# Optimization experiments

Hardware: AMD Instinct MI355X
Metric: run time of the kernel (lower is better)

Reference implementation:

```python
import jax, jax.numpy as jnp
import numpy as np

HIDDEN = 1024
B, S = 4, 2048


def setup_inputs() -> dict:
    key = jax.random.key(0)
    ks = jax.random.split(key, 8)
    scale = 1.0 / np.sqrt(HIDDEN)
    return {
        "hidden_states": jax.random.normal(ks[0], (B, S, HIDDEN), dtype=jnp.float32),
        "attention_mask": jnp.zeros((B, S, S), dtype=jnp.float32),
        "Wq": jax.random.normal(ks[1], (HIDDEN, HIDDEN), dtype=jnp.float32) * scale,
        "bq": jnp.zeros((HIDDEN,), dtype=jnp.float32),
        "Wk": jax.random.normal(ks[2], (HIDDEN, HIDDEN), dtype=jnp.float32) * scale,
        "bk": jnp.zeros((HIDDEN,), dtype=jnp.float32),
        "Wv": jax.random.normal(ks[3], (HIDDEN, HIDDEN), dtype=jnp.float32) * scale,
        "bv": jnp.zeros((HIDDEN,), dtype=jnp.float32),
    }


def reference(hidden_states, attention_mask, Wq, bq, Wk, bk, Wv, bv):
    # Dense projections (note: no head split in the original module)
    q = jnp.einsum('bsd,de->bse', hidden_states, Wq) + bq  # [B,S,H]
    k = jnp.einsum('bsd,de->bse', hidden_states, Wk) + bk
    v = jnp.einsum('bsd,de->bse', hidden_states, Wv) + bv
    # scores scaled by sqrt(hidden_size) (not per-head dim), per the source
    inv_scale = 1.0 / jnp.sqrt(jnp.asarray(q.shape[-1], dtype=q.dtype))
    scores = jnp.einsum('bqd,bkd->bqk', q, k) * inv_scale  # [B,S,S]
    scores = scores + attention_mask
    weights = jax.nn.softmax(scores, axis=-1)
    # dropout is identity (training=False)
    out = jnp.einsum('bqk,bkd->bqd', weights, v)  # [B,S,H]
    return out
```

## Files before the change

kernel.cpp:

```cpp
#include <hip/hip_runtime.h>
#include <stdint.h>

typedef __attribute__((ext_vector_type(8))) short short8;
typedef __attribute__((ext_vector_type(8))) unsigned short u16x8;
typedef __attribute__((ext_vector_type(4))) float f32x4;

__device__ __forceinline__ uint16_t f2bf(float x) {
  uint32_t u = __float_as_uint(x);
  uint32_t r = (u + 0x7FFFu + ((u >> 16) & 1u)) >> 16;
  return (uint16_t)r;
}
__device__ __forceinline__ float bf2f(uint16_t x) {
  return __uint_as_float(((uint32_t)x) << 16);
}

__device__ __forceinline__ void gl_lds16(const uint16_t* g, void* l) {
  __builtin_amdgcn_global_load_lds(
      (const __attribute__((address_space(1))) void*)g,
      (__attribute__((address_space(3))) void*)l, 16, 0, 0);
}


__global__ __launch_bounds__(256) void cvt_f32_to_bf16(const float* __restrict__ in,
                                                       uint16_t* __restrict__ out) {
  long i = ((long)blockIdx.x * 256 + threadIdx.x) * 8;
  f32x4 v0 = *(const f32x4*)(in + i);
  f32x4 v1 = *(const f32x4*)(in + i + 4);
  u16x8 o;
  o[0] = f2bf(v0[0]); o[1] = f2bf(v0[1]); o[2] = f2bf(v0[2]); o[3] = f2bf(v0[3]);
  o[4] = f2bf(v1[0]); o[5] = f2bf(v1[1]); o[6] = f2bf(v1[2]); o[7] = f2bf(v1[3]);
  *(u16x8*)(out + i) = o;
}

__global__ __launch_bounds__(64) void cvt_w_transpose(const float* __restrict__ W0,
                                                      const float* __restrict__ W1,
                                                      const float* __restrict__ W2,
                                                      uint16_t* __restrict__ WT) {
  const int z = blockIdx.z;
  const float* W = (z == 0) ? W0 : ((z == 1) ? W1 : W2);
  uint16_t* out = WT + (long)z * 1024 * 1024;
  const int n = blockIdx.x * 64 + threadIdx.x;
  const int k0 = blockIdx.y * 128;
  for (int kk = 0; kk < 128; kk += 8) {
    u16x8 o;
#pragma unroll
    for (int j = 0; j < 8; j++) o[j] = f2bf(W[(long)(k0 + kk + j) * 1024 + n]);
    *(u16x8*)(out + (long)n * 1024 + k0 + kk) = o;
  }
}

__global__ __launch_bounds__(256) void transpose_v(const uint16_t* __restrict__ V,
                                                   uint16_t* __restrict__ Vt) {
  __shared__ uint16_t tile[64][66];
  const int b = blockIdx.z;
  const int s0 = blockIdx.x * 64, d0 = blockIdx.y * 64;
  const int t = threadIdx.x;
  const int r = t >> 3, c = (t & 7) * 8;
  const uint16_t* Vb = V + (long)b * 2048 * 1024;
#pragma unroll
  for (int j = 0; j < 2; j++) {
    u16x8 v = *(const u16x8*)(Vb + (long)(s0 + r + 32 * j) * 1024 + d0 + c);
#pragma unroll
    for (int i = 0; i < 8; i++) tile[r + 32 * j][c + i] = v[i];
  }
  __syncthreads();
  uint16_t* Vtb = Vt + (long)b * 1024 * 2048;
#pragma unroll
  for (int j = 0; j < 2; j++) {
    const int d = r + 32 * j;
    u16x8 o;
#pragma unroll
    for (int i = 0; i < 8; i++) o[i] = tile[c + i][d];
    *(u16x8*)(Vtb + (long)(d0 + d) * 2048 + s0 + c) = o;
  }
}

template <int MODE, int AI>
__global__ __launch_bounds__(512, 2) void gemmX(
    const uint16_t* __restrict__ Abase, long sAz,
    const uint16_t* __restrict__ Bbase, long sBz,
    int K, int N,
    char* __restrict__ Cbase, long sCz,
    const float* __restrict__ e0, const float* __restrict__ e1,
    const float* __restrict__ e2,
    const float* __restrict__ maskb, long sMz, float scale,
    float* __restrict__ lsum) {
  constexpr int BM = AI * 32;
  constexpr int ABYTES = BM * 128;
  constexpr int BUFB = ABYTES + 32768;
  __shared__ __align__(16) char lds[2 * BUFB];
  const int t = threadIdx.x;
  const int lane = t & 63;
  const int w = t >> 6;
  const int bm = blockIdx.x, bn = blockIdx.y, bz = blockIdx.z;
  const uint16_t* A = (const uint16_t*)((const char*)Abase + (long)bz * sAz);
  const uint16_t* B = (const uint16_t*)((const char*)Bbase + (long)bz * sBz);

  const int srow = t >> 3;
  const int scol = ((((t & 7) * 16) ^ ((srow & 7) << 4)) >> 1);
  const uint16_t* gA[4];
  const uint16_t* gB[4];
#pragma unroll
  for (int s = 0; s < 4; s++) {
    gA[s] = A + (long)(bm * BM + (s % (AI / 2)) * 64 + srow) * K + scol;
    gB[s] = B + (long)(bn * 256 + s * 64 + srow) * K + scol;
  }

  const int wm = w >> 2, wn = w & 3;
  const int fr = lane & 15, kg = lane >> 4;
  const int X = (fr & 7) << 4;
  const int aRow = (wm * (AI * 16) + fr) * 128 + kg * 16;
  const int bRow = (wn * 64 + fr) * 128 + kg * 16;

  f32x4 acc[AI][4];
#pragma unroll
  for (int i = 0; i < AI; i++)
#pragma unroll
    for (int j = 0; j < 4; j++) acc[i][j] = (f32x4){0.f, 0.f, 0.f, 0.f};

  short8 aR[4][2], bR[4][2];
  const int NT = K >> 6;

#define ARD(off, i, ks) (*(const short8*)(lds + (off) + ((aRow + (i) * 2048 + (ks) * 64) ^ X)))
#define BRD(off, j, ks) (*(const short8*)(lds + ABYTES + (off) + ((bRow + (j) * 2048 + (ks) * 64) ^ X)))
#define STG_A01(off, ko) { gl_lds16(gA[0] + (ko), lds + (off) + w * 1024); \
                           gl_lds16(gA[1] + (ko), lds + (off) + 8192 + w * 1024); }
#define STG_A23(off, ko) { gl_lds16(gA[2] + (ko), lds + (off) + 16384 + w * 1024); \
                           gl_lds16(gA[3] + (ko), lds + (off) + 24576 + w * 1024); }
#define STG_B01(off, ko) { gl_lds16(gB[0] + (ko), lds + ABYTES + (off) + w * 1024); \
                           gl_lds16(gB[1] + (ko), lds + ABYTES + (off) + 8192 + w * 1024); }
#define STG_B23(off, ko) { gl_lds16(gB[2] + (ko), lds + ABYTES + (off) + 16384 + w * 1024); \
                           gl_lds16(gB[3] + (ko), lds + ABYTES + (off) + 24576 + w * 1024); }
#define LGKM0 { asm volatile("s_waitcnt lgkmcnt(0)" ::: "memory"); __builtin_amdgcn_sched_barrier(0); }
#define MFMA16(I0, J0)                                                            \
  __builtin_amdgcn_s_setprio(1);                                                  \
  _Pragma("unroll") for (int i = 0; i < 4; i++)                                   \
  _Pragma("unroll") for (int j = 0; j < 2; j++)                                   \
  _Pragma("unroll") for (int ks = 0; ks < 2; ks++)                                \
    acc[(I0) + i][(J0) + j] = __builtin_amdgcn_mfma_f32_16x16x32_bf16(            \
        aR[i][ks], bR[(J0) + j][ks], acc[(I0) + i][(J0) + j], 0, 0, 0);           \
  __builtin_amdgcn_s_setprio(0);

  if constexpr (AI == 8) { STG_A01(0, 0); STG_A23(0, 0); }
  else                   { STG_A01(0, 0); }
  STG_B01(0, 0); STG_B23(0, 0);

  int curo = 0;
  for (int tt = 0; tt < NT - 1; ++tt) {
    const int nxto = curo ^ BUFB;
    const int ko = (tt + 1) << 6;
    if constexpr (AI == 8) {
      STG_A01(nxto, ko);
      asm volatile("s_waitcnt vmcnt(2)" ::: "memory");
      __builtin_amdgcn_s_barrier();
      __builtin_amdgcn_sched_barrier(0);
#pragma unroll
      for (int i = 0; i < 4; i++) { aR[i][0] = ARD(curo, i, 0); aR[i][1] = ARD(curo, i, 1); }
#pragma unroll
      for (int j = 0; j < 4; j++) { bR[j][0] = BRD(curo, j, 0); bR[j][1] = BRD(curo, j, 1); }
      LGKM0;
      MFMA16(0, 0);
      __builtin_amdgcn_s_barrier();
      STG_A23(nxto, ko);
      __builtin_amdgcn_s_barrier();
      MFMA16(0, 2);
      __builtin_amdgcn_s_barrier();
      STG_B01(nxto, ko);
#pragma unroll
      for (int i = 0; i < 4; i++) { aR[i][0] = ARD(curo, 4 + i, 0); aR[i][1] = ARD(curo, 4 + i, 1); }
      __builtin_amdgcn_s_barrier();
      LGKM0;
      MFMA16(4, 2);
      __builtin_amdgcn_s_barrier();
      STG_B23(nxto, ko);
      __builtin_amdgcn_s_barrier();
      MFMA16(4, 0);
      __builtin_amdgcn_s_barrier();
    } else {
      STG_A01(nxto, ko);
      STG_B01(nxto, ko);
      asm volatile("s_waitcnt vmcnt(4)" ::: "memory");
      __builtin_amdgcn_s_barrier();
      __builtin_amdgcn_sched_barrier(0);
#pragma unroll
      for (int i = 0; i < 4; i++) { aR[i][0] = ARD(curo, i, 0); aR[i][1] = ARD(curo, i, 1); }
#pragma unroll
      for (int j = 0; j < 4; j++) { bR[j][0] = BRD(curo, j, 0); bR[j][1] = BRD(curo, j, 1); }
      LGKM0;
      MFMA16(0, 0);
      __builtin_amdgcn_s_barrier();
      STG_B23(nxto, ko);
      __builtin_amdgcn_s_barrier();
      MFMA16(0, 2);
      __builtin_amdgcn_s_barrier();
    }
    curo = nxto;
  }
  asm volatile("s_waitcnt vmcnt(0)" ::: "memory");
  __builtin_amdgcn_s_barrier();
  __builtin_amdgcn_sched_barrier(0);
#pragma unroll
  for (int i = 0; i < 4; i++) { aR[i][0] = ARD(curo, i, 0); aR[i][1] = ARD(curo, i, 1); }
#pragma unroll
  for (int j = 0; j < 4; j++) { bR[j][0] = BRD(curo, j, 0); bR[j][1] = BRD(curo, j, 1); }
  LGKM0;
  MFMA16(0, 0);
  MFMA16(0, 2);
  if constexpr (AI == 8) {
#pragma unroll
    for (int i = 0; i < 4; i++) { aR[i][0] = ARD(curo, 4 + i, 0); aR[i][1] = ARD(curo, 4 + i, 1); }
    LGKM0;
    MFMA16(4, 2);
    MFMA16(4, 0);
  }

  __syncthreads();
  constexpr int RS = 260;
  float* eL = (float*)lds;
  const int wboff = wm * (16 * RS) + (kg * 4) * RS + wn * 64 + fr;
  const int lr = t >> 4, slab = lr >> 4, row16 = lr & 15, cj = t & 15;
  const float* rb = eL + slab * (16 * RS) + row16 * RS + cj * 16;
  const int grow_base = bm * BM + slab * (AI * 16) + row16;

  f32x4 bias4[4];
  const uint16_t* Cu16 = nullptr;
  float* Cf32 = nullptr;
  uint16_t* Cw = nullptr;
  int colg = 0;
  const float* mk = nullptr;
  if constexpr (MODE == 0) {
    const int zz = bn >> 2;
    const float* bias = (zz == 0) ? e0 : ((zz == 1) ? e1 : e2);
    colg = (bn & 3) * 256 + cj * 16;
#pragma unroll
    for (int q = 0; q < 4; q++) bias4[q] = *(const f32x4*)(bias + colg + q * 4);
    Cw = (uint16_t*)(Cbase + (long)zz * sCz);
  } else if constexpr (MODE == 1) {
    colg = bn * 256 + cj * 16;
    Cw = (uint16_t*)(Cbase + (long)bz * sCz);
    mk = (const float*)((const char*)maskb + (long)bz * sMz);
  } else {
    colg = bn * 256 + cj * 16;
    Cf32 = (float*)(Cbase + (long)bz * sCz);
  }
  (void)Cu16;

#pragma unroll
  for (int i = 0; i < AI; i++) {
#pragma unroll
    for (int j = 0; j < 4; j++)
#pragma unroll
      for (int r = 0; r < 4; r++)
        eL[wboff + r * RS + j * 16] = acc[i][j][r];
    __syncthreads();
    f32x4 v0 = *(const f32x4*)(rb);
    f32x4 v1 = *(const f32x4*)(rb + 4);
    f32x4 v2 = *(const f32x4*)(rb + 8);
    f32x4 v3 = *(const f32x4*)(rb + 12);
    const int grow = grow_base + i * 16;
    if constexpr (MODE == 0) {
      v0 += bias4[0]; v1 += bias4[1]; v2 += bias4[2]; v3 += bias4[3];
      u16x8 o0, o1;
#pragma unroll
      for (int q = 0; q < 4; q++) {
        o0[q] = f2bf(v0[q]); o0[4 + q] = f2bf(v1[q]);
        o1[q] = f2bf(v2[q]); o1[4 + q] = f2bf(v3[q]);
      }
      uint16_t* dst = Cw + (long)grow * 1024 + colg;
      *(u16x8*)dst = o0;
      *(u16x8*)(dst + 8) = o1;
    } else if constexpr (MODE == 1) {
      const float* mrow = mk + (long)grow * N + colg;
      f32x4 m0 = *(const f32x4*)(mrow);
      f32x4 m1 = *(const f32x4*)(mrow + 4);
      f32x4 m2 = *(const f32x4*)(mrow + 8);
      f32x4 m3 = *(const f32x4*)(mrow + 12);
      float e[16];
#pragma unroll
      for (int q = 0; q < 4; q++) {
        e[q] = __expf(v0[q] * scale + m0[q]);
        e[4 + q] = __expf(v1[q] * scale + m1[q]);
        e[8 + q] = __expf(v2[q] * scale + m2[q]);
        e[12 + q] = __expf(v3[q] * scale + m3[q]);
      }
      float ps = 0.f;
#pragma unroll
      for (int q = 0; q < 16; q++) ps += e[q];
      ps += __shfl_xor(ps, 1);
      ps += __shfl_xor(ps, 2);
      ps += __shfl_xor(ps, 4);
      ps += __shfl_xor(ps, 8);
      if ((lane & 15) == 0) atomicAdd(lsum + (long)bz * 2048 + grow, ps);
      u16x8 o0, o1;
#pragma unroll
      for (int q = 0; q < 8; q++) { o0[q] = f2bf(e[q]); o1[q] = f2bf(e[8 + q]); }
      uint16_t* dst = Cw + (long)grow * N + colg;
      *(u16x8*)dst = o0;
      *(u16x8*)(dst + 8) = o1;
    } else {
      const float ri = 1.0f / lsum[(long)bz * 2048 + grow];
      v0 *= ri; v1 *= ri; v2 *= ri; v3 *= ri;
      float* dst = Cf32 + (long)grow * N + colg;
      *(f32x4*)dst = v0;
      *(f32x4*)(dst + 4) = v1;
      *(f32x4*)(dst + 8) = v2;
      *(f32x4*)(dst + 12) = v3;
    }
    __syncthreads();
  }
#undef ARD
#undef BRD
#undef STG_A01
#undef STG_A23
#undef STG_B01
#undef STG_B23
#undef LGKM0
#undef MFMA16
}

extern "C" void kernel_launch(void* const* d_in, const int* in_sizes, int n_in,
                              void* d_out, int out_size, void* d_ws, size_t ws_size,
                              hipStream_t stream) {
  const float* hs = (const float*)d_in[0];
  const float* mask = (const float*)d_in[1];
  const float* Wq = (const float*)d_in[2];
  const float* bq = (const float*)d_in[3];
  const float* Wk = (const float*)d_in[4];
  const float* bk = (const float*)d_in[5];
  const float* Wv = (const float*)d_in[6];
  const float* bv = (const float*)d_in[7];
  float* out = (float*)d_out;

  char* ws = (char*)d_ws;
  uint16_t* hsb = (uint16_t*)ws;
  uint16_t* WT = (uint16_t*)(ws + (16L << 20));
  uint16_t* QKV = (uint16_t*)(ws + (22L << 20));
  uint16_t* Vt = (uint16_t*)(ws + (70L << 20));
  uint16_t* E = (uint16_t*)(ws + (86L << 20));
  float* lsum = (float*)(ws + (118L << 20));

  cvt_f32_to_bf16<<<4096, 256, 0, stream>>>(hs, hsb);
  cvt_w_transpose<<<dim3(16, 8, 3), 64, 0, stream>>>(Wq, Wk, Wv, WT);
  hipMemsetAsync((void*)lsum, 0, 4L * 2048 * sizeof(float), stream);
  gemmX<0, 4><<<dim3(64, 12, 1), 512, 0, stream>>>(
      hsb, 0L, WT, 0L, 1024, 3072, (char*)QKV, 16L << 20,
      bq, bk, bv, nullptr, 0L, 0.f, nullptr);
  transpose_v<<<dim3(32, 16, 4), 256, 0, stream>>>(QKV + 2L * 8192 * 1024, Vt);
  gemmX<1, 8><<<dim3(8, 8, 4), 512, 0, stream>>>(
      QKV, 4L << 20, QKV + 8192L * 1024, 4L << 20, 1024, 2048, (char*)E, 8L << 20,
      nullptr, nullptr, nullptr, mask, 16L << 20, 0.03125f, lsum);
  gemmX<2, 4><<<dim3(16, 4, 4), 512, 0, stream>>>(
      E, 8L << 20, Vt, 4L << 20, 2048, 1024, (char*)out, 8L << 20,
      nullptr, nullptr, nullptr, nullptr, 0L, 0.f, lsum);
}
```

Baseline: 194.1 us.

## Replace hand-scheduled GEMM with simpler BK=32 k-major double-buffered kernel

Replaces the finely interleaved 64-wide-K GEMM pipeline (XOR-swizzled LDS, staged barriers, setprio) with a simpler kernel. It uses 32-wide K steps, a k-major LDS layout and one __syncthreads per step, and switches to 256-row M tiles with 256- or 128-column N tiles. Launch bounds now request 4 blocks per CU. The PV GEMM writes its output directly from registers with per-row normalization instead of staging through LDS. The aim is less pipeline complexity and higher occupancy. The cost is lost MFMA/load interleaving, likely LDS bank conflicts without swizzle, register pressure under a 4-block bound, and strided uncoalesced scalar stores in the final GEMM.

```diff
diff --git a/kernel.cpp b/kernel.cpp
--- a/kernel.cpp
+++ b/kernel.cpp
@@ -75,8 +75,8 @@
   }
 }
 
-template <int MODE, int AI>
-__global__ __launch_bounds__(512, 2) void gemmX(
+template <int MODE, int BN>
+__global__ __launch_bounds__(512, 4) void gemm2(
     const uint16_t* __restrict__ Abase, long sAz,
     const uint16_t* __restrict__ Bbase, long sBz,
     int K, int N,
@@ -85,9 +85,9 @@
     const float* __restrict__ e2,
     const float* __restrict__ maskb, long sMz, float scale,
     float* __restrict__ lsum) {
-  constexpr int BM = AI * 32;
-  constexpr int ABYTES = BM * 128;
-  constexpr int BUFB = ABYTES + 32768;
+  constexpr int ABYTES = 256 * 32 * 2;
+  constexpr int BBYTES = BN * 32 * 2;
+  constexpr int BUFB = ABYTES + BBYTES;
   __shared__ __align__(16) char lds[2 * BUFB];
   const int t = threadIdx.x;
   const int lane = t & 63;
@@ -96,122 +96,89 @@
   const uint16_t* A = (const uint16_t*)((const char*)Abase + (long)bz * sAz);
   const uint16_t* B = (const uint16_t*)((const char*)Bbase + (long)bz * sBz);
 
-  const int srow = t >> 3;
-  const int scol = ((((t & 7) * 16) ^ ((srow & 7) << 4)) >> 1);
-  const uint16_t* gA[4];
-  const uint16_t* gB[4];
-#pragma unroll
-  for (int s = 0; s < 4; s++) {
-    gA[s] = A + (long)(bm * BM + (s % (AI / 2)) * 64 + srow) * K + scol;
-    gB[s] = B + (long)(bn * 256 + s * 64 + srow) * K + scol;
-  }
-
-  const int wm = w >> 2, wn = w & 3;
+  const uint16_t* gA[2];
+#pragma unroll
+  for (int s = 0; s < 2; s++) {
+    const int li = s * 512 + t;
+    gA[s] = A + (long)(bm * 256 + (li & 255)) * K + (li >> 8) * 8;
+  }
+  const uint16_t* gB[2];
+  if constexpr (BN == 256) {
+#pragma unroll
+    for (int s = 0; s < 2; s++) {
+      const int li = s * 512 + t;
+      gB[s] = B + (long)(bn * 256 + (li & 255)) * K + (li >> 8) * 8;
+    }
+  } else {
+    gB[0] = B + (long)(bn * 128 + (t & 127)) * K + (t >> 7) * 8;
+    gB[1] = nullptr;
+  }
+
+  constexpr int NI = (BN == 256) ? 8 : 4;
+  const int wm = (BN == 256) ? (w >> 2) : (w >> 1);
+  const int wn = (BN == 256) ? (w & 3) : (w & 1);
   const int fr = lane & 15, kg = lane >> 4;
-  const int X = (fr & 7) << 4;
-  const int aRow = (wm * (AI * 16) + fr) * 128 + kg * 16;
-  const int bRow = (wn * 64 + fr) * 128 + kg * 16;
-
-  f32x4 acc[AI][4];
-#pragma unroll
-  for (int i = 0; i < AI; i++)
+
+  const int aBase = kg * 4096 + (wm * (NI * 16) + fr) * 16;
+  const int bBase = kg * (BN * 16) + (wn * 64 + fr) * 16;
+
+  f32x4 acc[NI][4];
+#pragma unroll
+  for (int i = 0; i < NI; i++)
 #pragma unroll
     for (int j = 0; j < 4; j++) acc[i][j] = (f32x4){0.f, 0.f, 0.f, 0.f};
 
-  short8 aR[4][2], bR[4][2];
-  const int NT = K >> 6;
-
-#define ARD(off, i, ks) (*(const short8*)(lds + (off) + ((aRow + (i) * 2048 + (ks) * 64) ^ X)))
-#define BRD(off, j, ks) (*(const short8*)(lds + ABYTES + (off) + ((bRow + (j) * 2048 + (ks) * 64) ^ X)))
-#define STG_A01(off, ko) { gl_lds16(gA[0] + (ko), lds + (off) + w * 1024); \
-                           gl_lds16(gA[1] + (ko), lds + (off) + 8192 + w * 1024); }
-#define STG_A23(off, ko) { gl_lds16(gA[2] + (ko), lds + (off) + 16384 + w * 1024); \
-                           gl_lds16(gA[3] + (ko), lds + (off) + 24576 + w * 1024); }
-#define STG_B01(off, ko) { gl_lds16(gB[0] + (ko), lds + ABYTES + (off) + w * 1024); \
-                           gl_lds16(gB[1] + (ko), lds + ABYTES + (off) + 8192 + w * 1024); }
-#define STG_B23(off, ko) { gl_lds16(gB[2] + (ko), lds + ABYTES + (off) + 16384 + w * 1024); \
-                           gl_lds16(gB[3] + (ko), lds + ABYTES + (off) + 24576 + w * 1024); }
-#define LGKM0 { asm volatile("s_waitcnt lgkmcnt(0)" ::: "memory"); __builtin_amdgcn_sched_barrier(0); }
-#define MFMA16(I0, J0)                                                            \
-  __builtin_amdgcn_s_setprio(1);                                                  \
-  _Pragma("unroll") for (int i = 0; i < 4; i++)                                   \
-  _Pragma("unroll") for (int j = 0; j < 2; j++)                                   \
-  _Pragma("unroll") for (int ks = 0; ks < 2; ks++)                                \
-    acc[(I0) + i][(J0) + j] = __builtin_amdgcn_mfma_f32_16x16x32_bf16(            \
-        aR[i][ks], bR[(J0) + j][ks], acc[(I0) + i][(J0) + j], 0, 0, 0);           \
-  __builtin_amdgcn_s_setprio(0);
-
-  if constexpr (AI == 8) { STG_A01(0, 0); STG_A23(0, 0); }
-  else                   { STG_A01(0, 0); }
-  STG_B01(0, 0); STG_B23(0, 0);
-
-  int curo = 0;
-  for (int tt = 0; tt < NT - 1; ++tt) {
-    const int nxto = curo ^ BUFB;
-    const int ko = (tt + 1) << 6;
-    if constexpr (AI == 8) {
-      STG_A01(nxto, ko);
-      asm volatile("s_waitcnt vmcnt(2)" ::: "memory");
-      __builtin_amdgcn_s_barrier();
-      __builtin_amdgcn_sched_barrier(0);
-#pragma unroll
-      for (int i = 0; i < 4; i++) { aR[i][0] = ARD(curo, i, 0); aR[i][1] = ARD(curo, i, 1); }
-#pragma unroll
-      for (int j = 0; j < 4; j++) { bR[j][0] = BRD(curo, j, 0); bR[j][1] = BRD(curo, j, 1); }
-      LGKM0;
-      MFMA16(0, 0);
-      __builtin_amdgcn_s_barrier();
-      STG_A23(nxto, ko);
-      __builtin_amdgcn_s_barrier();
-      MFMA16(0, 2);
-      __builtin_amdgcn_s_barrier();
-      STG_B01(nxto, ko);
-#pragma unroll
-      for (int i = 0; i < 4; i++) { aR[i][0] = ARD(curo, 4 + i, 0); aR[i][1] = ARD(curo, 4 + i, 1); }
-      __builtin_amdgcn_s_barrier();
-      LGKM0;
-      MFMA16(4, 2);
-      __builtin_amdgcn_s_barrier();
-      STG_B23(nxto, ko);
-      __builtin_amdgcn_s_barrier();
-      MFMA16(4, 0);
-      __builtin_amdgcn_s_barrier();
-    } else {
-      STG_A01(nxto, ko);
-      STG_B01(nxto, ko);
-      asm volatile("s_waitcnt vmcnt(4)" ::: "memory");
-      __builtin_amdgcn_s_barrier();
-      __builtin_amdgcn_sched_barrier(0);
-#pragma unroll
-      for (int i = 0; i < 4; i++) { aR[i][0] = ARD(curo, i, 0); aR[i][1] = ARD(curo, i, 1); }
-#pragma unroll
-      for (int j = 0; j < 4; j++) { bR[j][0] = BRD(curo, j, 0); bR[j][1] = BRD(curo, j, 1); }
-      LGKM0;
-      MFMA16(0, 0);
-      __builtin_amdgcn_s_barrier();
-      STG_B23(nxto, ko);
-      __builtin_amdgcn_s_barrier();
-      MFMA16(0, 2);
-      __builtin_amdgcn_s_barrier();
+#define STG_A(off, ko) { gl_lds16(gA[0] + (ko), lds + (off) + w * 1024); \
+                         gl_lds16(gA[1] + (ko), lds + (off) + 8192 + w * 1024); }
+#define STG_B(off, ko) { gl_lds16(gB[0] + (ko), lds + ABYTES + (off) + w * 1024); \
+                         if (BN == 256) gl_lds16(gB[1] + (ko), lds + ABYTES + (off) + 8192 + w * 1024); }
+
+  STG_A(0, 0); STG_B(0, 0);
+
+  int cur = 0;
+  for (int k0 = 0; k0 < K; k0 += 32) {
+    __syncthreads();
+    if (k0 + 32 < K) {
+      const int nb = (cur ^ 1) * BUFB, kn = k0 + 32;
+      STG_A(nb, kn); STG_B(nb, kn);
     }
-    curo = nxto;
-  }
-  asm volatile("s_waitcnt vmcnt(0)" ::: "memory");
-  __builtin_amdgcn_s_barrier();
-  __builtin_amdgcn_sched_barrier(0);
-#pragma unroll
-  for (int i = 0; i < 4; i++) { aR[i][0] = ARD(curo, i, 0); aR[i][1] = ARD(curo, i, 1); }
-#pragma unroll
-  for (int j = 0; j < 4; j++) { bR[j][0] = BRD(curo, j, 0); bR[j][1] = BRD(curo, j, 1); }
-  LGKM0;
-  MFMA16(0, 0);
-  MFMA16(0, 2);
-  if constexpr (AI == 8) {
-#pragma unroll
-    for (int i = 0; i < 4; i++) { aR[i][0] = ARD(curo, 4 + i, 0); aR[i][1] = ARD(curo, 4 + i, 1); }
-    LGKM0;
-    MFMA16(4, 2);
-    MFMA16(4, 0);
+    const char* Ab = lds + cur * BUFB;
+    const char* Bb = lds + cur * BUFB + ABYTES;
+    short8 a[NI], b[4];
+#pragma unroll
+    for (int i = 0; i < NI; i++) a[i] = *(const short8*)(Ab + aBase + i * 256);
+#pragma unroll
+    for (int j = 0; j < 4; j++) b[j] = *(const short8*)(Bb + bBase + j * 256);
+#pragma unroll
+    for (int i = 0; i < NI; i++)
+#pragma unroll
+      for (int j = 0; j < 4; j++)
+        acc[i][j] = __builtin_amdgcn_mfma_f32_16x16x32_bf16(a[i], b[j], acc[i][j], 0, 0, 0);
+    cur ^= 1;
+  }
+#undef STG_A
+#undef STG_B
+
+  if constexpr (MODE == 2) {
+    const int row0 = bm * 256 + wm * 64 + (kg << 2);
+    const int col0 = bn * 128 + wn * 64 + fr;
+    float* C = (float*)(Cbase + (long)bz * sCz);
+    const float* ls = lsum + (long)bz * 2048;
+#pragma unroll
+    for (int i = 0; i < NI; i++) {
+      const int rr = row0 + i * 16;
+      const float ri0 = 1.0f / ls[rr], ri1 = 1.0f / ls[rr + 1];
+      const float ri2 = 1.0f / ls[rr + 2], ri3 = 1.0f / ls[rr + 3];
+#pragma unroll
+      for (int j = 0; j < 4; j++) {
+        float* dst = C + (long)rr * N + col0 + j * 16;
+        dst[0] = acc[i][j][0] * ri0;
+        dst[(long)N] = acc[i][j][1] * ri1;
+        dst[(long)2 * N] = acc[i][j][2] * ri2;
+        dst[(long)3 * N] = acc[i][j][3] * ri3;
+      }
+    }
+    return;
   }
 
   __syncthreads();
@@ -220,11 +187,9 @@
   const int wboff = wm * (16 * RS) + (kg * 4) * RS + wn * 64 + fr;
   const int lr = t >> 4, slab = lr >> 4, row16 = lr & 15, cj = t & 15;
   const float* rb = eL + slab * (16 * RS) + row16 * RS + cj * 16;
-  const int grow_base = bm * BM + slab * (AI * 16) + row16;
+  const int grow_base = bm * 256 + slab * 128 + row16;
 
   f32x4 bias4[4];
-  const uint16_t* Cu16 = nullptr;
-  float* Cf32 = nullptr;
   uint16_t* Cw = nullptr;
   int colg = 0;
   const float* mk = nullptr;
@@ -235,18 +200,14 @@
 #pragma unroll
     for (int q = 0; q < 4; q++) bias4[q] = *(const f32x4*)(bias + colg + q * 4);
     Cw = (uint16_t*)(Cbase + (long)zz * sCz);
-  } else if constexpr (MODE == 1) {
+  } else {
     colg = bn * 256 + cj * 16;
     Cw = (uint16_t*)(Cbase + (long)bz * sCz);
     mk = (const float*)((const char*)maskb + (long)bz * sMz);
-  } else {
-    colg = bn * 256 + cj * 16;
-    Cf32 = (float*)(Cbase + (long)bz * sCz);
-  }
-  (void)Cu16;
-
-#pragma unroll
-  for (int i = 0; i < AI; i++) {
+  }
+
+#pragma unroll
+  for (int i = 0; i < 8; i++) {
 #pragma unroll
     for (int j = 0; j < 4; j++)
 #pragma unroll
@@ -269,7 +230,7 @@
       uint16_t* dst = Cw + (long)grow * 1024 + colg;
       *(u16x8*)dst = o0;
       *(u16x8*)(dst + 8) = o1;
-    } else if constexpr (MODE == 1) {
+    } else {
       const float* mrow = mk + (long)grow * N + colg;
       f32x4 m0 = *(const f32x4*)(mrow);
       f32x4 m1 = *(const f32x4*)(mrow + 4);
@@ -297,25 +258,9 @@
       uint16_t* dst = Cw + (long)grow * N + colg;
       *(u16x8*)dst = o0;
       *(u16x8*)(dst + 8) = o1;
-    } else {
-      const float ri = 1.0f / lsum[(long)bz * 2048 + grow];
-      v0 *= ri; v1 *= ri; v2 *= ri; v3 *= ri;
-      float* dst = Cf32 + (long)grow * N + colg;
-      *(f32x4*)dst = v0;
-      *(f32x4*)(dst + 4) = v1;
-      *(f32x4*)(dst + 8) = v2;
-      *(f32x4*)(dst + 12) = v3;
     }
     __syncthreads();
   }
-#undef ARD
-#undef BRD
-#undef STG_A01
-#undef STG_A23
-#undef STG_B01
-#undef STG_B23
-#undef LGKM0
-#undef MFMA16
 }
 
 extern "C" void kernel_launch(void* const* d_in, const int* in_sizes, int n_in,
@@ -342,14 +287,14 @@
   cvt_f32_to_bf16<<<4096, 256, 0, stream>>>(hs, hsb);
   cvt_w_transpose<<<dim3(16, 8, 3), 64, 0, stream>>>(Wq, Wk, Wv, WT);
   hipMemsetAsync((void*)lsum, 0, 4L * 2048 * sizeof(float), stream);
-  gemmX<0, 4><<<dim3(64, 12, 1), 512, 0, stream>>>(
+  gemm2<0, 256><<<dim3(32, 12, 1), 512, 0, stream>>>(
       hsb, 0L, WT, 0L, 1024, 3072, (char*)QKV, 16L << 20,
       bq, bk, bv, nullptr, 0L, 0.f, nullptr);
   transpose_v<<<dim3(32, 16, 4), 256, 0, stream>>>(QKV + 2L * 8192 * 1024, Vt);
-  gemmX<1, 8><<<dim3(8, 8, 4), 512, 0, stream>>>(
+  gemm2<1, 256><<<dim3(8, 8, 4), 512, 0, stream>>>(
       QKV, 4L << 20, QKV + 8192L * 1024, 4L << 20, 1024, 2048, (char*)E, 8L << 20,
       nullptr, nullptr, nullptr, mask, 16L << 20, 0.03125f, lsum);
-  gemmX<2, 4><<<dim3(16, 4, 4), 512, 0, stream>>>(
+  gemm2<2, 128><<<dim3(8, 8, 4), 512, 0, stream>>>(
       E, 8L << 20, Vt, 4L << 20, 2048, 1024, (char*)out, 8L << 20,
       nullptr, nullptr, nullptr, nullptr, 0L, 0.f, lsum);
 }
```

Result: slower. 687.0 us (+254.0%).
